# Kernel tuning notes

Measured on AMD Instinct MI355X. Metric: run time of the kernel, lower is better.

Reference implementation:

```python
import jax, jax.numpy as jnp
import numpy as np

N = 100000
E = 3200000
NFEAT = 256
NHID = 128
NCLASS = 16
TEXT_CNT = 50000


def setup_inputs() -> dict:
    key = jax.random.key(0)
    ks = jax.random.split(key, 12)
    x = jax.random.normal(ks[0], (N, NFEAT), dtype=jnp.float32)
    adj_rows = jax.random.randint(ks[1], (E,), 0, N, dtype=jnp.int32)
    adj_cols = jax.random.randint(ks[2], (E,), 0, N, dtype=jnp.int32)
    # positive normalized-adjacency-like weights (~1/avg_degree scale)
    adj_vals = jax.random.uniform(ks[3], (E,), dtype=jnp.float32) / 32.0
    W1 = jax.random.normal(ks[4], (NFEAT, NHID), dtype=jnp.float32) / np.sqrt(NFEAT)
    b1 = jax.random.normal(ks[5], (NHID,), dtype=jnp.float32) * 0.01
    W2 = jax.random.normal(ks[6], (NHID, NFEAT), dtype=jnp.float32) / np.sqrt(NHID)
    b2 = jax.random.normal(ks[7], (NFEAT,), dtype=jnp.float32) * 0.01
    cW1 = jax.random.normal(ks[8], (NFEAT, NCLASS), dtype=jnp.float32) / np.sqrt(NFEAT)
    cb1 = jax.random.normal(ks[9], (NCLASS,), dtype=jnp.float32) * 0.01
    cW2 = jax.random.normal(ks[10], (NFEAT, NCLASS), dtype=jnp.float32) / np.sqrt(NFEAT)
    cb2 = jax.random.normal(ks[11], (NCLASS,), dtype=jnp.float32) * 0.01
    return {"x": x, "adj_rows": adj_rows, "adj_cols": adj_cols, "adj_vals": adj_vals,
            "W1": W1, "b1": b1, "W2": W2, "b2": b2,
            "cW1": cW1, "cb1": cb1, "cW2": cw2 if (cw2 := None) else cW2, "cb2": cb2}


def spmm(rows, cols, vals, dense):
    # out[r] = sum_{e: rows[e]==r} vals[e] * dense[cols[e]]   (COO SpMM)
    gathered = vals[:, None] * dense[cols]  # [E, D]
    return jax.ops.segment_sum(gathered, rows, num_segments=N)


def reference(x, adj_rows, adj_cols, adj_vals, W1, b1, W2, b2, cW1, cb1, cW2, cb2):
    # gc1: adj @ (x @ W1) + b1, then ReLU (dropout is identity at inference)
    h = jax.nn.relu(spmm(adj_rows, adj_cols, adj_vals, x @ W1) + b1)  # [N, NHID]
    # gc2: adj @ (h @ W2) + b2
    out = spmm(adj_rows, adj_cols, adj_vals, h @ W2) + b2  # [N, NFEAT]
    text_cls = out[:TEXT_CNT] @ cW1 + cb1  # [TEXT_CNT, NCLASS]
    img_cls = out[TEXT_CNT:] @ cW2 + cb2   # [N-TEXT_CNT, NCLASS]
    return (out, text_cls, img_cls)
```

## Files before the change

### kernel.cpp

```cpp
#include <hip/hip_runtime.h>

#define N_NODES  100000
#define N_EDGES  3200000
#define NFEAT    256
#define NHID     128
#define NCLASS   16
#define TEXT_CNT 50000

#define RPB      256
#define NB       ((N_NODES + RPB - 1) / RPB)
#define CAP      16384
#define S_EPT    32
#define NBLKS    ((N_EDGES + 256 * S_EPT - 1) / (256 * S_EPT))
#define GEMM_LDS (2 * 128 * 40 * 2)

typedef unsigned int uint;
typedef __bf16 bf16x8 __attribute__((ext_vector_type(8)));
typedef __bf16 bf16x4 __attribute__((ext_vector_type(4)));
typedef float f32x4 __attribute__((ext_vector_type(4)));

__device__ inline uint bf16_rne(float f) {
  uint u = __float_as_uint(f);
  return (u + 0x7fffu + ((u >> 16) & 1u)) >> 16;
}
__device__ inline float bf_lo(uint u) { return __uint_as_float(u << 16); }
__device__ inline float bf_hi(uint u) { return __uint_as_float(u & 0xffff0000u); }


__global__ __launch_bounds__(256) void prep_kernel(const float* __restrict__ W1,
                                                   const float* __restrict__ W2,
                                                   const float* __restrict__ b2,
                                                   const float* __restrict__ cW1,
                                                   const float* __restrict__ cb1,
                                                   const float* __restrict__ cW2,
                                                   const float* __restrict__ cb2,
                                                   unsigned short* __restrict__ W1t,
                                                   unsigned short* __restrict__ W2t,
                                                   float* __restrict__ Wc1, float* __restrict__ bc1,
                                                   float* __restrict__ Wc2, float* __restrict__ bc2,
                                                   int* __restrict__ gcursor) {
  int idx = blockIdx.x * 256 + threadIdx.x;
  if (idx < 32768) {
    int n = idx >> 8, k = idx & 255;
    W1t[idx] = (unsigned short)bf16_rne(W1[(size_t)k * NHID + n]);
  } else if (idx < 65536) {
    int i2 = idx - 32768;
    int n = i2 >> 7, k = i2 & 127;
    W2t[i2] = (unsigned short)bf16_rne(W2[(size_t)k * NFEAT + n]);
  } else if (idx < 69632) {
    int e = idx - 65536;
    int set = e >> 11;
    int e2 = e & 2047;
    int i = e2 >> 4, c = e2 & 15;
    const float* cw = set ? cW2 : cW1;
    float acc = 0.f;
    for (int k = 0; k < NFEAT; ++k)
      acc += W2[(size_t)i * NFEAT + k] * cw[k * NCLASS + c];
    (set ? Wc2 : Wc1)[e2] = acc;
    if (e < 32) {
      int s2 = e >> 4, c2 = e & 15;
      const float* cwb = s2 ? cW2 : cW1;
      float b = (s2 ? cb2 : cb1)[c2];
      for (int k = 0; k < NFEAT; ++k) b += b2[k] * cwb[k * NCLASS + c2];
      (s2 ? bc2 : bc1)[c2] = b;
    }
  } else if (idx < 69632 + NB) {
    int b = idx - 69632;
    gcursor[b] = b * CAP;
  }
}


__device__ __forceinline__ void scatter_body(int bx, const int* __restrict__ rows,
                                             const int* __restrict__ cols,
                                             const float* __restrict__ vals,
                                             int* __restrict__ gcursor,
                                             int2* __restrict__ packed, int E,
                                             int* __restrict__ smem) {
  int* hist = smem;
  int* cur = smem + NB;
  for (int i = threadIdx.x; i < NB; i += 256) hist[i] = 0;
  __syncthreads();
  int base = bx * (256 * S_EPT);
#pragma unroll
  for (int i = 0; i < S_EPT; ++i) {
    int e = base + i * 256 + threadIdx.x;
    if (e < E) atomicAdd(&hist[rows[e] >> 8], 1);
  }
  __syncthreads();
  for (int i = threadIdx.x; i < NB; i += 256) {
    int h = hist[i];
    cur[i] = h ? atomicAdd(&gcursor[i], h) : 0;
  }
  __syncthreads();
#pragma unroll
  for (int i = 0; i < S_EPT; ++i) {
    int e = base + i * 256 + threadIdx.x;
    if (e < E) {
      int r = rows[e];
      int b = r >> 8;
      int p = atomicAdd(&cur[b], 1);
      if (p < ((b + 1) << 14))
        packed[p] = make_int2(((r & 255) << 17) | cols[e], __float_as_int(vals[e]));
    }
  }
}


template <int A_FP32, int OUT_BF16, int K, int N>
__device__ __forceinline__ void gemm_body(int bx, int by, const void* __restrict__ Aptr,
                                          const __bf16* __restrict__ Bt,
                                          const float* __restrict__ bias,
                                          void* __restrict__ Cptr, int M,
                                          __bf16* __restrict__ As, __bf16* __restrict__ Bs) {
  int tid = threadIdx.x;
  int lane = tid & 63;
  int w = tid >> 6;
  int wr = w >> 1, wc = w & 1;
  int brow = bx * 128;
  int bcol = by * 128;
  int r16 = lane & 15, kb = lane >> 4;

  f32x4 acc[4][4];
#pragma unroll
  for (int m = 0; m < 4; ++m)
#pragma unroll
    for (int n = 0; n < 4; ++n) acc[m][n] = (f32x4){0.f, 0.f, 0.f, 0.f};

  for (int k0 = 0; k0 < K; k0 += 32) {
    if (A_FP32) {
      const float* A = (const float*)Aptr;
#pragma unroll
      for (int i = 0; i < 4; ++i) {
        int idx = tid + i * 256;
        int row = idx >> 3;
        int kq = (idx & 7) << 2;
        int gr = brow + row;
        float4 v = make_float4(0.f, 0.f, 0.f, 0.f);
        if (gr < M) v = *(const float4*)&A[(size_t)gr * K + k0 + kq];
        bf16x4 o;
        o[0] = (__bf16)v.x; o[1] = (__bf16)v.y; o[2] = (__bf16)v.z; o[3] = (__bf16)v.w;
        *(bf16x4*)&As[row * 40 + kq] = o;
      }
    } else {
      const __bf16* A = (const __bf16*)Aptr;
#pragma unroll
      for (int i = 0; i < 2; ++i) {
        int idx = tid + i * 256;
        int row = idx >> 2;
        int kq = (idx & 3) << 3;
        int gr = brow + row;
        bf16x8 v = {};
        if (gr < M) v = *(const bf16x8*)&A[(size_t)gr * K + k0 + kq];
        *(bf16x8*)&As[row * 40 + kq] = v;
      }
    }
#pragma unroll
    for (int i = 0; i < 2; ++i) {
      int idx = tid + i * 256;
      int col = idx >> 2;
      int kq = (idx & 3) << 3;
      bf16x8 v = *(const bf16x8*)&Bt[(size_t)(bcol + col) * K + k0 + kq];
      *(bf16x8*)&Bs[col * 40 + kq] = v;
    }
    __syncthreads();

    bf16x8 a[4], b[4];
#pragma unroll
    for (int m = 0; m < 4; ++m)
      a[m] = *(bf16x8*)&As[(wr * 64 + m * 16 + r16) * 40 + kb * 8];
#pragma unroll
    for (int n = 0; n < 4; ++n)
      b[n] = *(bf16x8*)&Bs[(wc * 64 + n * 16 + r16) * 40 + kb * 8];
#pragma unroll
    for (int m = 0; m < 4; ++m)
#pragma unroll
      for (int n = 0; n < 4; ++n)
        acc[m][n] = __builtin_amdgcn_mfma_f32_16x16x32_bf16(a[m], b[n], acc[m][n], 0, 0, 0);
    __syncthreads();
  }

  int crow0 = brow + wr * 64;
  int ccol0 = bcol + wc * 64;
#pragma unroll
  for (int n = 0; n < 4; ++n) {
    int col = ccol0 + n * 16 + r16;
    float bv = bias ? bias[col] : 0.f;
#pragma unroll
    for (int m = 0; m < 4; ++m) {
#pragma unroll
      for (int r = 0; r < 4; ++r) {
        int row = crow0 + m * 16 + kb * 4 + r;
        if (row < M) {
          float val = acc[m][n][r] + bv;
          if (OUT_BF16)
            ((unsigned short*)Cptr)[(size_t)row * N + col] = (unsigned short)bf16_rne(val);
          else
            ((float*)Cptr)[(size_t)row * N + col] = val;
        }
      }
    }
  }
}


__global__ __launch_bounds__(256) void fused_sg1_kernel(
    const int* __restrict__ rows, const int* __restrict__ cols, const float* __restrict__ vals,
    int* __restrict__ gcursor, int2* __restrict__ packedA, int E,
    const float* __restrict__ x, const __bf16* __restrict__ W1t, uint* __restrict__ t1u, int M) {
  extern __shared__ __align__(16) char dynbuf[];
  if (blockIdx.x < NBLKS)
    scatter_body(blockIdx.x, rows, cols, vals, gcursor, packedA, E, (int*)dynbuf);
  else
    gemm_body<1, 1, NFEAT, NHID>(blockIdx.x - NBLKS, 0, x, W1t, nullptr, t1u, M,
                                 (__bf16*)dynbuf, (__bf16*)dynbuf + 128 * 40);
}


__global__ __launch_bounds__(512) void csr_finalize_kernel(const int* __restrict__ gcursor,
                                                           const int2* __restrict__ packed_in,
                                                           int2* __restrict__ packed_out,
                                                           int* __restrict__ row_ptr) {
  __shared__ int pre[512];
  __shared__ int hist[RPB];
  __shared__ int cur[RPB];
  int b = blockIdx.x;
  int t = threadIdx.x;
  int cntt = (t < NB) ? (gcursor[t] - t * CAP) : 0;
  pre[t] = cntt;
  __syncthreads();
  for (int off = 1; off < 512; off <<= 1) {
    int u = (t >= off) ? pre[t - off] : 0;
    __syncthreads();
    pre[t] += u;
    __syncthreads();
  }
  int cnt = gcursor[b] - b * CAP;
  int gout = pre[b] - cnt;
  int s0 = b * CAP;
  int end = s0 + cnt;
  if (t < RPB) hist[t] = 0;
  __syncthreads();
  {
    int i = s0 + t;
    for (; i + 1536 < end; i += 2048) {
      int2 a0 = packed_in[i], a1 = packed_in[i + 512];
      int2 a2 = packed_in[i + 1024], a3 = packed_in[i + 1536];
      atomicAdd(&hist[a0.x >> 17], 1);
      atomicAdd(&hist[a1.x >> 17], 1);
      atomicAdd(&hist[a2.x >> 17], 1);
      atomicAdd(&hist[a3.x >> 17], 1);
    }
    for (; i < end; i += 512) atomicAdd(&hist[packed_in[i].x >> 17], 1);
  }
  __syncthreads();
  int v = (t < RPB) ? hist[t] : 0;
  if (t < RPB) cur[t] = v;
  __syncthreads();
  for (int off = 1; off < RPB; off <<= 1) {
    int u = (t >= off && t < RPB) ? cur[t - off] : 0;
    __syncthreads();
    if (t < RPB) cur[t] += u;
    __syncthreads();
  }
  if (t < RPB) {
    int rbase = gout + cur[t] - v;
    int row = b * RPB + t;
    if (row < N_NODES) row_ptr[row] = rbase;
    cur[t] = rbase;
  }
  if (b == 0 && t == 0) row_ptr[N_NODES] = N_EDGES;
  __syncthreads();
  {
    int i = s0 + t;
    for (; i + 1536 < end; i += 2048) {
      int2 a0 = packed_in[i], a1 = packed_in[i + 512];
      int2 a2 = packed_in[i + 1024], a3 = packed_in[i + 1536];
      int p0 = atomicAdd(&cur[a0.x >> 17], 1);
      int p1 = atomicAdd(&cur[a1.x >> 17], 1);
      int p2 = atomicAdd(&cur[a2.x >> 17], 1);
      int p3 = atomicAdd(&cur[a3.x >> 17], 1);
      packed_out[p0] = make_int2((a0.x & 0x1FFFF) << 8, a0.y);
      packed_out[p1] = make_int2((a1.x & 0x1FFFF) << 8, a1.y);
      packed_out[p2] = make_int2((a2.x & 0x1FFFF) << 8, a2.y);
      packed_out[p3] = make_int2((a3.x & 0x1FFFF) << 8, a3.y);
    }
    for (; i < end; i += 512) {
      int2 pk = packed_in[i];
      int p = atomicAdd(&cur[pk.x >> 17], 1);
      packed_out[p] = make_int2((pk.x & 0x1FFFF) << 8, pk.y);
    }
  }
}


__global__ __launch_bounds__(256) void spmm_bf16_kernel(const int* __restrict__ row_ptr,
                                                        const int2* __restrict__ packed,
                                                        const uint* __restrict__ src,
                                                        uint* __restrict__ dst,
                                                        const float* __restrict__ bias,
                                                        int relu, int nrows) {
  int tid = threadIdx.x;
  int lane = tid & 63;
  int half = lane >> 5;
  int l32 = lane & 31;
  int row = blockIdx.x * 4 + (tid >> 6);
  if (row >= nrows) return;
  int s = row_ptr[row];
  int e = row_ptr[row + 1];
  const char* srcb = (const char*)src + (l32 << 3);
  float a0 = 0.f, a1 = 0.f, a2 = 0.f, a3 = 0.f;
  int i = s;
  for (; i + 16 <= e; i += 16) {
    int2 m0 = packed[i + 0 + half], m1 = packed[i + 2 + half];
    int2 m2 = packed[i + 4 + half], m3 = packed[i + 6 + half];
    int2 m4 = packed[i + 8 + half], m5 = packed[i + 10 + half];
    int2 m6 = packed[i + 12 + half], m7 = packed[i + 14 + half];
    uint2 u0 = *(const uint2*)(srcb + (uint)m0.x);
    uint2 u1 = *(const uint2*)(srcb + (uint)m1.x);
    uint2 u2 = *(const uint2*)(srcb + (uint)m2.x);
    uint2 u3 = *(const uint2*)(srcb + (uint)m3.x);
    uint2 u4 = *(const uint2*)(srcb + (uint)m4.x);
    uint2 u5 = *(const uint2*)(srcb + (uint)m5.x);
    uint2 u6 = *(const uint2*)(srcb + (uint)m6.x);
    uint2 u7 = *(const uint2*)(srcb + (uint)m7.x);
    float v0 = __int_as_float(m0.y), v1 = __int_as_float(m1.y);
    float v2 = __int_as_float(m2.y), v3 = __int_as_float(m3.y);
    float v4 = __int_as_float(m4.y), v5 = __int_as_float(m5.y);
    float v6 = __int_as_float(m6.y), v7 = __int_as_float(m7.y);
    a0 += v0 * bf_lo(u0.x); a1 += v0 * bf_hi(u0.x); a2 += v0 * bf_lo(u0.y); a3 += v0 * bf_hi(u0.y);
    a0 += v1 * bf_lo(u1.x); a1 += v1 * bf_hi(u1.x); a2 += v1 * bf_lo(u1.y); a3 += v1 * bf_hi(u1.y);
    a0 += v2 * bf_lo(u2.x); a1 += v2 * bf_hi(u2.x); a2 += v2 * bf_lo(u2.y); a3 += v2 * bf_hi(u2.y);
    a0 += v3 * bf_lo(u3.x); a1 += v3 * bf_hi(u3.x); a2 += v3 * bf_lo(u3.y); a3 += v3 * bf_hi(u3.y);
    a0 += v4 * bf_lo(u4.x); a1 += v4 * bf_hi(u4.x); a2 += v4 * bf_lo(u4.y); a3 += v4 * bf_hi(u4.y);
    a0 += v5 * bf_lo(u5.x); a1 += v5 * bf_hi(u5.x); a2 += v5 * bf_lo(u5.y); a3 += v5 * bf_hi(u5.y);
    a0 += v6 * bf_lo(u6.x); a1 += v6 * bf_hi(u6.x); a2 += v6 * bf_lo(u6.y); a3 += v6 * bf_hi(u6.y);
    a0 += v7 * bf_lo(u7.x); a1 += v7 * bf_hi(u7.x); a2 += v7 * bf_lo(u7.y); a3 += v7 * bf_hi(u7.y);
  }
  for (; i + 8 <= e; i += 8) {
    int2 m0 = packed[i + 0 + half], m1 = packed[i + 2 + half];
    int2 m2 = packed[i + 4 + half], m3 = packed[i + 6 + half];
    uint2 u0 = *(const uint2*)(srcb + (uint)m0.x);
    uint2 u1 = *(const uint2*)(srcb + (uint)m1.x);
    uint2 u2 = *(const uint2*)(srcb + (uint)m2.x);
    uint2 u3 = *(const uint2*)(srcb + (uint)m3.x);
    float v0 = __int_as_float(m0.y), v1 = __int_as_float(m1.y);
    float v2 = __int_as_float(m2.y), v3 = __int_as_float(m3.y);
    a0 += v0 * bf_lo(u0.x); a1 += v0 * bf_hi(u0.x); a2 += v0 * bf_lo(u0.y); a3 += v0 * bf_hi(u0.y);
    a0 += v1 * bf_lo(u1.x); a1 += v1 * bf_hi(u1.x); a2 += v1 * bf_lo(u1.y); a3 += v1 * bf_hi(u1.y);
    a0 += v2 * bf_lo(u2.x); a1 += v2 * bf_hi(u2.x); a2 += v2 * bf_lo(u2.y); a3 += v2 * bf_hi(u2.y);
    a0 += v3 * bf_lo(u3.x); a1 += v3 * bf_hi(u3.x); a2 += v3 * bf_lo(u3.y); a3 += v3 * bf_hi(u3.y);
  }
  for (; i + 4 <= e; i += 4) {
    int2 m0 = packed[i + 0 + half], m1 = packed[i + 2 + half];
    uint2 u0 = *(const uint2*)(srcb + (uint)m0.x);
    uint2 u1 = *(const uint2*)(srcb + (uint)m1.x);
    float v0 = __int_as_float(m0.y), v1 = __int_as_float(m1.y);
    a0 += v0 * bf_lo(u0.x); a1 += v0 * bf_hi(u0.x); a2 += v0 * bf_lo(u0.y); a3 += v0 * bf_hi(u0.y);
    a0 += v1 * bf_lo(u1.x); a1 += v1 * bf_hi(u1.x); a2 += v1 * bf_lo(u1.y); a3 += v1 * bf_hi(u1.y);
  }
  for (; i < e; i += 2) {
    int ee = i + half;
    int ok = ee < e;
    int2 m = packed[ok ? ee : (e - 1)];
    uint2 u = *(const uint2*)(srcb + (uint)m.x);
    float v = ok ? __int_as_float(m.y) : 0.f;
    a0 += v * bf_lo(u.x); a1 += v * bf_hi(u.x); a2 += v * bf_lo(u.y); a3 += v * bf_hi(u.y);
  }
  a0 += __shfl_xor(a0, 32); a1 += __shfl_xor(a1, 32);
  a2 += __shfl_xor(a2, 32); a3 += __shfl_xor(a3, 32);
  if (half == 0) {
    if (bias) {
      a0 += bias[4 * l32 + 0]; a1 += bias[4 * l32 + 1];
      a2 += bias[4 * l32 + 2]; a3 += bias[4 * l32 + 3];
    }
    if (relu) {
      a0 = fmaxf(a0, 0.f); a1 = fmaxf(a1, 0.f);
      a2 = fmaxf(a2, 0.f); a3 = fmaxf(a3, 0.f);
    }
    uint2 o;
    o.x = bf16_rne(a0) | (bf16_rne(a1) << 16);
    o.y = bf16_rne(a2) | (bf16_rne(a3) << 16);
    *(uint2*)&dst[(size_t)row * 64 + l32 * 2] = o;
  }
}


template <int A_FP32, int OUT_BF16, int K, int N>
__global__ __launch_bounds__(256) void gemm_mfma_kernel(const void* __restrict__ Aptr,
                                                        const __bf16* __restrict__ Bt,
                                                        const float* __restrict__ bias,
                                                        void* __restrict__ Cptr, int M) {
  __shared__ __align__(16) __bf16 smem[2 * 128 * 40];
  gemm_body<A_FP32, OUT_BF16, K, N>(blockIdx.x, blockIdx.y, Aptr, Bt, bias, Cptr, M,
                                    smem, smem + 128 * 40);
}


__global__ __launch_bounds__(256) void cls_kernel(const uint* __restrict__ t3,
                                                  const float* __restrict__ Wc1,
                                                  const float* __restrict__ bc1,
                                                  const float* __restrict__ Wc2,
                                                  const float* __restrict__ bc2,
                                                  float* __restrict__ out1,
                                                  float* __restrict__ out2) {
  int half = gridDim.x >> 1;
  int region = blockIdx.x >= half;
  int bid = region ? blockIdx.x - half : blockIdx.x;
  const float* Wc = region ? Wc2 : Wc1;
  const float* bc = region ? bc2 : bc1;
  float* outp = region ? out2 : out1;
  int row0 = region ? TEXT_CNT : 0;
  int nrows = region ? (N_NODES - TEXT_CNT) : TEXT_CNT;

  int lane = threadIdx.x & 63;
  int wav = bid * 4 + (threadIdx.x >> 6);
  int nw = half * 4;
  int c = lane & 15;
  int kg = lane >> 4;
  float w[32];
#pragma unroll
  for (int j = 0; j < 32; ++j) w[j] = Wc[(kg * 32 + j) * NCLASS + c];
  float bcv = bc[c];
  for (int r = wav; r < nrows; r += nw) {
    const uint4* rp = (const uint4*)&t3[(size_t)(row0 + r) * 64 + kg * 16];
    float acc = 0.f;
#pragma unroll
    for (int q = 0; q < 4; ++q) {
      uint4 u = rp[q];
      acc += bf_lo(u.x) * w[q * 8 + 0] + bf_hi(u.x) * w[q * 8 + 1]
           + bf_lo(u.y) * w[q * 8 + 2] + bf_hi(u.y) * w[q * 8 + 3]
           + bf_lo(u.z) * w[q * 8 + 4] + bf_hi(u.z) * w[q * 8 + 5]
           + bf_lo(u.w) * w[q * 8 + 6] + bf_hi(u.w) * w[q * 8 + 7];
    }
    acc += __shfl_xor(acc, 16);
    acc += __shfl_xor(acc, 32);
    if (lane < 16) outp[(size_t)r * NCLASS + lane] = acc + bcv;
  }
}


extern "C" void kernel_launch(void* const* d_in, const int* in_sizes, int n_in,
                              void* d_out, int out_size, void* d_ws, size_t ws_size,
                              hipStream_t stream) {
  const float* x     = (const float*)d_in[0];
  const int*   arows = (const int*)d_in[1];
  const int*   acols = (const int*)d_in[2];
  const float* avals = (const float*)d_in[3];
  const float* W1    = (const float*)d_in[4];
  const float* b1    = (const float*)d_in[5];
  const float* W2    = (const float*)d_in[6];
  const float* b2    = (const float*)d_in[7];
  const float* cW1   = (const float*)d_in[8];
  const float* cb1   = (const float*)d_in[9];
  const float* cW2   = (const float*)d_in[10];
  const float* cb2   = (const float*)d_in[11];
  float* outp = (float*)d_out;

  char* ws = (char*)d_ws;
  size_t off = 0;
  auto alloc = [&](size_t bytes) -> void* {
    void* p = ws + off;
    off += (bytes + 255) & ~(size_t)255;
    return p;
  };
  uint*  t1u     = (uint*) alloc((size_t)N_NODES * 64 * 4);
  uint*  hu      = (uint*) alloc((size_t)N_NODES * 64 * 4);
  uint*  t3u     = (uint*) alloc((size_t)N_NODES * 64 * 4);
  int2*  packedA = (int2*) alloc((size_t)NB * CAP * 8);
  int2*  packedB = (int2*) alloc((size_t)N_EDGES * 8);
  int*   gcursor = (int*)  alloc((size_t)NB * 4);
  int*   rowp    = (int*)  alloc((size_t)(N_NODES + 1) * 4);
  unsigned short* W1t = (unsigned short*)alloc((size_t)NHID * NFEAT * 2);
  unsigned short* W2t = (unsigned short*)alloc((size_t)NFEAT * NHID * 2);
  float* Wc1     = (float*)alloc(NHID * NCLASS * 4);
  float* Wc2     = (float*)alloc(NHID * NCLASS * 4);
  float* bc1     = (float*)alloc(64);
  float* bc2     = (float*)alloc(64);

  prep_kernel<<<(69632 + NB + 255) / 256, 256, 0, stream>>>(
      W1, W2, b2, cW1, cb1, cW2, cb2, W1t, W2t, Wc1, bc1, Wc2, bc2, gcursor);

  int mblk = (N_NODES + 127) / 128;
  fused_sg1_kernel<<<NBLKS + mblk, 256, GEMM_LDS, stream>>>(
      arows, acols, avals, gcursor, packedA, N_EDGES,
      x, (const __bf16*)W1t, t1u, N_NODES);

  csr_finalize_kernel<<<NB, 512, 0, stream>>>(gcursor, packedA, packedB, rowp);

  spmm_bf16_kernel<<<(N_NODES + 3) / 4, 256, 0, stream>>>(rowp, packedB, t1u, hu, b1, 1, N_NODES);
  spmm_bf16_kernel<<<(N_NODES + 3) / 4, 256, 0, stream>>>(rowp, packedB, hu, t3u, nullptr, 0, N_NODES);
  gemm_mfma_kernel<0, 0, NHID, NFEAT><<<dim3(mblk, 2), 256, 0, stream>>>(
      t3u, (const __bf16*)W2t, b2, outp, N_NODES);
  cls_kernel<<<2048, 256, 0, stream>>>(t3u, Wc1, bc1, Wc2, bc2,
      outp + (size_t)N_NODES * NFEAT,
      outp + (size_t)N_NODES * NFEAT + (size_t)TEXT_CNT * NCLASS);
}
```

Baseline: 445.2 us.

## Stage scatter and CSR finalize through LDS, unfuse gemm1, fuse gemm2 with classifier

The scatter kernel now bucket-sorts each 8192-edge chunk in LDS with a local prefix scan, then writes each bucket contiguously to global memory. This replaces the per-edge random global writes. CSR finalize likewise sorts each bucket in LDS before a coalesced write-out, falling back to direct scatter when a bucket overflows. The first GEMM is split back out of the fused scatter launch, and the second GEMM and the classifier now share one launch. The extra LDS use (about 64KB+ per block) lowers occupancy for the sort kernels.

After: 428.2 us. 1.04x faster.

```diff
diff --git a/kernel.cpp b/kernel.cpp
--- a/kernel.cpp
+++ b/kernel.cpp
@@ -10,9 +10,9 @@
 #define RPB      256
 #define NB       ((N_NODES + RPB - 1) / RPB)
 #define CAP      16384
-#define S_EPT    32
-#define NBLKS    ((N_EDGES + 256 * S_EPT - 1) / (256 * S_EPT))
-#define GEMM_LDS (2 * 128 * 40 * 2)
+#define SC_EDGES 8192
+#define SC_BLKS  ((N_EDGES + SC_EDGES - 1) / SC_EDGES)
+#define FN_CAPL  9216
 
 typedef unsigned int uint;
 typedef __bf16 bf16x8 __attribute__((ext_vector_type(8)));
@@ -71,37 +71,128 @@
 }
 
 
-__device__ __forceinline__ void scatter_body(int bx, const int* __restrict__ rows,
-                                             const int* __restrict__ cols,
-                                             const float* __restrict__ vals,
-                                             int* __restrict__ gcursor,
-                                             int2* __restrict__ packed, int E,
-                                             int* __restrict__ smem) {
-  int* hist = smem;
-  int* cur = smem + NB;
-  for (int i = threadIdx.x; i < NB; i += 256) hist[i] = 0;
-  __syncthreads();
-  int base = bx * (256 * S_EPT);
-#pragma unroll
-  for (int i = 0; i < S_EPT; ++i) {
-    int e = base + i * 256 + threadIdx.x;
+__global__ __launch_bounds__(512) void scatter_sort_kernel(const int* __restrict__ rows,
+                                                           const int* __restrict__ cols,
+                                                           const float* __restrict__ vals,
+                                                           int* __restrict__ gcursor,
+                                                           int2* __restrict__ packedA, int E) {
+  __shared__ int2 eds[SC_EDGES];
+  __shared__ int hist[512];
+  __shared__ int bcnt[NB];
+  __shared__ int lofs[NB];
+  __shared__ int lcur[NB];
+  __shared__ int gofs[NB];
+  int t = threadIdx.x;
+  int base = blockIdx.x * SC_EDGES;
+  hist[t] = 0;
+  __syncthreads();
+#pragma unroll
+  for (int i = 0; i < SC_EDGES / 512; ++i) {
+    int e = base + i * 512 + t;
     if (e < E) atomicAdd(&hist[rows[e] >> 8], 1);
   }
   __syncthreads();
-  for (int i = threadIdx.x; i < NB; i += 256) {
-    int h = hist[i];
-    cur[i] = h ? atomicAdd(&gcursor[i], h) : 0;
-  }
-  __syncthreads();
-#pragma unroll
-  for (int i = 0; i < S_EPT; ++i) {
-    int e = base + i * 256 + threadIdx.x;
+  int v = hist[t];
+  if (t < NB) bcnt[t] = v;
+  __syncthreads();
+  for (int off = 1; off < 512; off <<= 1) {
+    int u = (t >= off) ? hist[t - off] : 0;
+    __syncthreads();
+    hist[t] += u;
+    __syncthreads();
+  }
+  if (t < NB) {
+    int ex = hist[t] - v;
+    lofs[t] = ex;
+    lcur[t] = ex;
+    gofs[t] = v ? atomicAdd(&gcursor[t], v) : 0;
+  }
+  __syncthreads();
+#pragma unroll
+  for (int i = 0; i < SC_EDGES / 512; ++i) {
+    int e = base + i * 512 + t;
     if (e < E) {
       int r = rows[e];
       int b = r >> 8;
-      int p = atomicAdd(&cur[b], 1);
-      if (p < ((b + 1) << 14))
-        packed[p] = make_int2(((r & 255) << 17) | cols[e], __float_as_int(vals[e]));
+      int p = atomicAdd(&lcur[b], 1);
+      eds[p] = make_int2(((r & 255) << 17) | cols[e], __float_as_int(vals[e]));
+    }
+  }
+  __syncthreads();
+  int wid = t >> 6, lane = t & 63;
+  for (int b = wid; b < NB; b += 8) {
+    int cnt = bcnt[b];
+    int lo = lofs[b];
+    int go = gofs[b];
+    int lim = (b + 1) << 14;
+    for (int j = lane; j < cnt; j += 64)
+      if (go + j < lim) packedA[go + j] = eds[lo + j];
+  }
+}
+
+
+__global__ __launch_bounds__(512) void csr_finalize_kernel(const int* __restrict__ gcursor,
+                                                           const int2* __restrict__ packedA,
+                                                           int2* __restrict__ packedB,
+                                                           int* __restrict__ row_ptr) {
+  __shared__ int2 eds[FN_CAPL];
+  __shared__ int pre[512];
+  __shared__ int rh[RPB];
+  __shared__ int rofs[RPB];
+  __shared__ int rcur[RPB];
+  int b = blockIdx.x;
+  int t = threadIdx.x;
+  int cntt = (t < NB) ? (gcursor[t] - t * CAP) : 0;
+  pre[t] = cntt;
+  __syncthreads();
+  for (int off = 1; off < 512; off <<= 1) {
+    int u = (t >= off) ? pre[t - off] : 0;
+    __syncthreads();
+    pre[t] += u;
+    __syncthreads();
+  }
+  int cnt = gcursor[b] - b * CAP;
+  int gout = pre[b] - cnt;
+  int s0 = b * CAP;
+  int end = s0 + cnt;
+  if (t < RPB) rh[t] = 0;
+  __syncthreads();
+  for (int i = s0 + t; i < end; i += 512)
+    atomicAdd(&rh[packedA[i].x >> 17], 1);
+  __syncthreads();
+  int v = (t < RPB) ? rh[t] : 0;
+  if (t < RPB) rofs[t] = v;
+  __syncthreads();
+  for (int off = 1; off < RPB; off <<= 1) {
+    int u = (t >= off && t < RPB) ? rofs[t - off] : 0;
+    __syncthreads();
+    if (t < RPB) rofs[t] += u;
+    __syncthreads();
+  }
+  if (t < RPB) {
+    int ex = rofs[t] - v;
+    rcur[t] = ex;
+    int row = b * RPB + t;
+    if (row < N_NODES) row_ptr[row] = gout + ex;
+  }
+  if (b == 0 && t == 0) row_ptr[N_NODES] = N_EDGES;
+  __syncthreads();
+  if (cnt <= FN_CAPL) {
+    for (int i = s0 + t; i < end; i += 512) {
+      int2 pk = packedA[i];
+      int p = atomicAdd(&rcur[pk.x >> 17], 1);
+      eds[p] = pk;
+    }
+    __syncthreads();
+    for (int i = t; i < cnt; i += 512) {
+      int2 pk = eds[i];
+      packedB[gout + i] = make_int2((pk.x & 0x1FFFF) << 8, pk.y);
+    }
+  } else {
+    for (int i = s0 + t; i < end; i += 512) {
+      int2 pk = packedA[i];
+      int p = atomicAdd(&rcur[pk.x >> 17], 1);
+      packedB[gout + p] = make_int2((pk.x & 0x1FFFF) << 8, pk.y);
     }
   }
 }
@@ -204,93 +295,14 @@
 }
 
 
-__global__ __launch_bounds__(256) void fused_sg1_kernel(
-    const int* __restrict__ rows, const int* __restrict__ cols, const float* __restrict__ vals,
-    int* __restrict__ gcursor, int2* __restrict__ packedA, int E,
-    const float* __restrict__ x, const __bf16* __restrict__ W1t, uint* __restrict__ t1u, int M) {
-  extern __shared__ __align__(16) char dynbuf[];
-  if (blockIdx.x < NBLKS)
-    scatter_body(blockIdx.x, rows, cols, vals, gcursor, packedA, E, (int*)dynbuf);
-  else
-    gemm_body<1, 1, NFEAT, NHID>(blockIdx.x - NBLKS, 0, x, W1t, nullptr, t1u, M,
-                                 (__bf16*)dynbuf, (__bf16*)dynbuf + 128 * 40);
-}
-
-
-__global__ __launch_bounds__(512) void csr_finalize_kernel(const int* __restrict__ gcursor,
-                                                           const int2* __restrict__ packed_in,
-                                                           int2* __restrict__ packed_out,
-                                                           int* __restrict__ row_ptr) {
-  __shared__ int pre[512];
-  __shared__ int hist[RPB];
-  __shared__ int cur[RPB];
-  int b = blockIdx.x;
-  int t = threadIdx.x;
-  int cntt = (t < NB) ? (gcursor[t] - t * CAP) : 0;
-  pre[t] = cntt;
-  __syncthreads();
-  for (int off = 1; off < 512; off <<= 1) {
-    int u = (t >= off) ? pre[t - off] : 0;
-    __syncthreads();
-    pre[t] += u;
-    __syncthreads();
-  }
-  int cnt = gcursor[b] - b * CAP;
-  int gout = pre[b] - cnt;
-  int s0 = b * CAP;
-  int end = s0 + cnt;
-  if (t < RPB) hist[t] = 0;
-  __syncthreads();
-  {
-    int i = s0 + t;
-    for (; i + 1536 < end; i += 2048) {
-      int2 a0 = packed_in[i], a1 = packed_in[i + 512];
-      int2 a2 = packed_in[i + 1024], a3 = packed_in[i + 1536];
-      atomicAdd(&hist[a0.x >> 17], 1);
-      atomicAdd(&hist[a1.x >> 17], 1);
-      atomicAdd(&hist[a2.x >> 17], 1);
-      atomicAdd(&hist[a3.x >> 17], 1);
-    }
-    for (; i < end; i += 512) atomicAdd(&hist[packed_in[i].x >> 17], 1);
-  }
-  __syncthreads();
-  int v = (t < RPB) ? hist[t] : 0;
-  if (t < RPB) cur[t] = v;
-  __syncthreads();
-  for (int off = 1; off < RPB; off <<= 1) {
-    int u = (t >= off && t < RPB) ? cur[t - off] : 0;
-    __syncthreads();
-    if (t < RPB) cur[t] += u;
-    __syncthreads();
-  }
-  if (t < RPB) {
-    int rbase = gout + cur[t] - v;
-    int row = b * RPB + t;
-    if (row < N_NODES) row_ptr[row] = rbase;
-    cur[t] = rbase;
-  }
-  if (b == 0 && t == 0) row_ptr[N_NODES] = N_EDGES;
-  __syncthreads();
-  {
-    int i = s0 + t;
-    for (; i + 1536 < end; i += 2048) {
-      int2 a0 = packed_in[i], a1 = packed_in[i + 512];
-      int2 a2 = packed_in[i + 1024], a3 = packed_in[i + 1536];
-      int p0 = atomicAdd(&cur[a0.x >> 17], 1);
-      int p1 = atomicAdd(&cur[a1.x >> 17], 1);
-      int p2 = atomicAdd(&cur[a2.x >> 17], 1);
-      int p3 = atomicAdd(&cur[a3.x >> 17], 1);
-      packed_out[p0] = make_int2((a0.x & 0x1FFFF) << 8, a0.y);
-      packed_out[p1] = make_int2((a1.x & 0x1FFFF) << 8, a1.y);
-      packed_out[p2] = make_int2((a2.x & 0x1FFFF) << 8, a2.y);
-      packed_out[p3] = make_int2((a3.x & 0x1FFFF) << 8, a3.y);
-    }
-    for (; i < end; i += 512) {
-      int2 pk = packed_in[i];
-      int p = atomicAdd(&cur[pk.x >> 17], 1);
-      packed_out[p] = make_int2((pk.x & 0x1FFFF) << 8, pk.y);
-    }
-  }
+template <int A_FP32, int OUT_BF16, int K, int N>
+__global__ __launch_bounds__(256) void gemm_mfma_kernel(const void* __restrict__ Aptr,
+                                                        const __bf16* __restrict__ Bt,
+                                                        const float* __restrict__ bias,
+                                                        void* __restrict__ Cptr, int M) {
+  __shared__ __align__(16) __bf16 smem[2 * 128 * 40];
+  gemm_body<A_FP32, OUT_BF16, K, N>(blockIdx.x, blockIdx.y, Aptr, Bt, bias, Cptr, M,
+                                    smem, smem + 128 * 40);
 }
 
 
@@ -386,27 +398,17 @@
 }
 
 
-template <int A_FP32, int OUT_BF16, int K, int N>
-__global__ __launch_bounds__(256) void gemm_mfma_kernel(const void* __restrict__ Aptr,
-                                                        const __bf16* __restrict__ Bt,
-                                                        const float* __restrict__ bias,
-                                                        void* __restrict__ Cptr, int M) {
-  __shared__ __align__(16) __bf16 smem[2 * 128 * 40];
-  gemm_body<A_FP32, OUT_BF16, K, N>(blockIdx.x, blockIdx.y, Aptr, Bt, bias, Cptr, M,
-                                    smem, smem + 128 * 40);
-}
-
-
-__global__ __launch_bounds__(256) void cls_kernel(const uint* __restrict__ t3,
-                                                  const float* __restrict__ Wc1,
-                                                  const float* __restrict__ bc1,
-                                                  const float* __restrict__ Wc2,
-                                                  const float* __restrict__ bc2,
-                                                  float* __restrict__ out1,
-                                                  float* __restrict__ out2) {
-  int half = gridDim.x >> 1;
-  int region = blockIdx.x >= half;
-  int bid = region ? blockIdx.x - half : blockIdx.x;
+__device__ __forceinline__ void cls_body(int bid, int clsblks,
+                                         const uint* __restrict__ t3,
+                                         const float* __restrict__ Wc1,
+                                         const float* __restrict__ bc1,
+                                         const float* __restrict__ Wc2,
+                                         const float* __restrict__ bc2,
+                                         float* __restrict__ out1,
+                                         float* __restrict__ out2) {
+  int half = clsblks >> 1;
+  int region = bid >= half;
+  int b = region ? bid - half : bid;
   const float* Wc = region ? Wc2 : Wc1;
   const float* bc = region ? bc2 : bc1;
   float* outp = region ? out2 : out1;
@@ -414,7 +416,7 @@
   int nrows = region ? (N_NODES - TEXT_CNT) : TEXT_CNT;
 
   int lane = threadIdx.x & 63;
-  int wav = bid * 4 + (threadIdx.x >> 6);
+  int wav = b * 4 + (threadIdx.x >> 6);
   int nw = half * 4;
   int c = lane & 15;
   int kg = lane >> 4;
@@ -436,6 +438,29 @@
     acc += __shfl_xor(acc, 16);
     acc += __shfl_xor(acc, 32);
     if (lane < 16) outp[(size_t)r * NCLASS + lane] = acc + bcv;
+  }
+}
+
+
+__global__ __launch_bounds__(256) void fused_g2c_kernel(const uint* __restrict__ t3u,
+                                                        const __bf16* __restrict__ W2t,
+                                                        const float* __restrict__ b2,
+                                                        float* __restrict__ outp,
+                                                        const float* __restrict__ Wc1,
+                                                        const float* __restrict__ bc1,
+                                                        const float* __restrict__ Wc2,
+                                                        const float* __restrict__ bc2,
+                                                        float* __restrict__ out1,
+                                                        float* __restrict__ out2,
+                                                        int g2blks, int clsblks) {
+  __shared__ __align__(16) __bf16 smem[2 * 128 * 40];
+  if ((int)blockIdx.x < g2blks) {
+    int bx = blockIdx.x >> 1;
+    int by = blockIdx.x & 1;
+    gemm_body<0, 0, NHID, NFEAT>(bx, by, t3u, W2t, b2, outp, N_NODES,
+                                 smem, smem + 128 * 40);
+  } else {
+    cls_body(blockIdx.x - g2blks, clsblks, t3u, Wc1, bc1, Wc2, bc2, out1, out2);
   }
 }
 
@@ -481,18 +506,20 @@
   prep_kernel<<<(69632 + NB + 255) / 256, 256, 0, stream>>>(
       W1, W2, b2, cW1, cb1, cW2, cb2, W1t, W2t, Wc1, bc1, Wc2, bc2, gcursor);
 
+  scatter_sort_kernel<<<SC_BLKS, 512, 0, stream>>>(arows, acols, avals, gcursor, packedA, N_EDGES);
+
+  csr_finalize_kernel<<<NB, 512, 0, stream>>>(gcursor, packedA, packedB, rowp);
+
   int mblk = (N_NODES + 127) / 128;
-  fused_sg1_kernel<<<NBLKS + mblk, 256, GEMM_LDS, stream>>>(
-      arows, acols, avals, gcursor, packedA, N_EDGES,
-      x, (const __bf16*)W1t, t1u, N_NODES);
-
-  csr_finalize_kernel<<<NB, 512, 0, stream>>>(gcursor, packedA, packedB, rowp);
-
+  gemm_mfma_kernel<1, 1, NFEAT, NHID><<<dim3(mblk, 1), 256, 0, stream>>>(
+      x, (const __bf16*)W1t, nullptr, t1u, N_NODES);
   spmm_bf16_kernel<<<(N_NODES + 3) / 4, 256, 0, stream>>>(rowp, packedB, t1u, hu, b1, 1, N_NODES);
   spmm_bf16_kernel<<<(N_NODES + 3) / 4, 256, 0, stream>>>(rowp, packedB, hu, t3u, nullptr, 0, N_NODES);
-  gemm_mfma_kernel<0, 0, NHID, NFEAT><<<dim3(mblk, 2), 256, 0, stream>>>(
-      t3u, (const __bf16*)W2t, b2, outp, N_NODES);
-  cls_kernel<<<2048, 256, 0, stream>>>(t3u, Wc1, bc1, Wc2, bc2,
+  int g2blks = mblk * 2;
+  int clsblks = 2048;
+  fused_g2c_kernel<<<g2blks + clsblks, 256, 0, stream>>>(
+      t3u, (const __bf16*)W2t, b2, outp, Wc1, bc1, Wc2, bc2,
       outp + (size_t)N_NODES * NFEAT,
-      outp + (size_t)N_NODES * NFEAT + (size_t)TEXT_CNT * NCLASS);
-}
+      outp + (size_t)N_NODES * NFEAT + (size_t)TEXT_CNT * NCLASS,
+      g2blks, clsblks);
+}
```
